# Optimization experiments

Measured on AMD Instinct MI355X. Metric: run time of the kernel, lower is better.

## Reference

```python
import jax, jax.numpy as jnp
import numpy as np

STAGE = 100  # number of weight bins


def _bin_reconstruct(w, affine):
    # Faithful vectorization of the 100-iter binning loop: element in bin i
    # (half-open interval) gets scaled by affine[i]; the max element falls
    # outside every bin (w < wmin + stage*range/stage fails) and is zeroed.
    flat = w.reshape(-1)
    wmin, wmax = flat.min(), flat.max()
    idx = jnp.floor((flat - wmin) / (wmax - wmin) * STAGE).astype(jnp.int32)
    mask = (idx < STAGE).astype(flat.dtype)  # mask is detached in torch (non-diff anyway)
    scale = affine[jnp.clip(idx, 0, STAGE - 1)]
    return flat * scale * mask


def _kl_vs_laplace(new_flat, lap):
    # F.kl_div(log_softmax(w), softmax(lap), reduction='none').mean()
    logq = jax.nn.log_softmax(new_flat)
    p = jax.nn.softmax(lap)
    return (p * (jnp.log(p) - logq)).mean()


def _adder2d(x, w, stride, padding, groups=1):
    # AdderNet conv: out = -sum_k |patch_k - w_k| (no bias)
    O, Cg, kh, kw = w.shape
    patches = jax.lax.conv_general_dilated_patches(
        x, (kh, kw), (stride, stride), [(padding, padding), (padding, padding)])
    B, _, Hp, Wp = patches.shape  # channel dim ordered (C, kh, kw), C-major
    if groups == 1:
        p = patches.reshape(B, 1, Cg * kh * kw, Hp, Wp)
        wf = w.reshape(1, O, Cg * kh * kw, 1, 1)
    else:  # depthwise: groups == C_in, Cg == 1, O == C_in
        p = patches.reshape(B, O, kh * kw, Hp, Wp)
        wf = w.reshape(1, O, kh * kw, 1, 1)
    return -jnp.abs(p - wf).sum(axis=2)  # [B, O, Hp, Wp]


def _bn_train(x, g, b, eps=1e-5):
    # BatchNorm2d in training mode (batch statistics, biased variance)
    m = x.mean(axis=(0, 2, 3), keepdims=True)
    v = ((x - m) ** 2).mean(axis=(0, 2, 3), keepdims=True)
    return (x - m) * jax.lax.rsqrt(v + eps) * g.reshape(1, -1, 1, 1) + b.reshape(1, -1, 1, 1)


def _forward(x, sw_ds, sw_c1, sw_c2, sw_c3, a_ds, a_c1, a_c2, a_c3, peg_w,
             g1, b1, g2, b2, g3, b3, gds, bds, lap_ds, lap_c1, lap_c2, lap_c3):
    kl = jnp.float32(0.0)
    f_ds = _bin_reconstruct(sw_ds, a_ds)
    kl = kl + _kl_vs_laplace(f_ds, lap_ds)
    f_c1 = _bin_reconstruct(sw_c1, a_c1)
    kl = kl + _kl_vs_laplace(f_c1, lap_c1)
    residual = jax.nn.relu(_bn_train(_adder2d(x, f_ds.reshape(sw_ds.shape), 1, 0), gds, bds))
    h = _adder2d(x, f_c1.reshape(sw_c1.shape), 1, 0)
    h = _adder2d(h, peg_w, 1, 1, groups=peg_w.shape[0])  # PEG depthwise 3x3
    h = jax.nn.relu(_bn_train(h, g1, b1))
    f_c2 = _bin_reconstruct(sw_c2, a_c2)
    kl = kl + _kl_vs_laplace(f_c2, lap_c2)
    h = _adder2d(h, f_c2.reshape(sw_c2.shape), 1, 1)
    h = jax.nn.relu(_bn_train(h, g2, b2))
    f_c3 = _bin_reconstruct(sw_c3, a_c3)
    kl = kl + _kl_vs_laplace(f_c3, lap_c3)
    h = _adder2d(h, f_c3.reshape(sw_c3.shape), 1, 0)
    h = _bn_train(h, g3, b3)  # bn3 gamma zero-initialized
    return jax.nn.relu(h + residual), kl


def setup_inputs() -> dict:
    key = jax.random.key(0)
    ks = jax.random.split(key, 16)
    inp = {
        'x': jax.random.normal(ks[0], (4, 128, 28, 28), jnp.float32),
        'sw_downsample': jax.random.normal(ks[1], (256, 128, 1, 1), jnp.float32) * 0.05,
        'sw_conv1': jax.random.normal(ks[2], (64, 128, 1, 1), jnp.float32) * 0.05,
        'sw_conv2': jax.random.normal(ks[3], (64, 64, 3, 3), jnp.float32) * 0.05,
        'sw_conv3': jax.random.normal(ks[4], (256, 64, 1, 1), jnp.float32) * 0.05,
        'downsample_affine': jax.random.normal(ks[5], (100,), jnp.float32),
        'conv1_affine': jax.random.normal(ks[6], (100,), jnp.float32),
        'conv2_affine': jax.random.normal(ks[7], (100,), jnp.float32),
        'conv3_affine': jax.random.normal(ks[8], (100,), jnp.float32),
        'peg_w': jax.random.normal(ks[9], (64, 1, 3, 3), jnp.float32) * 0.05,
        'bn1_g': jnp.ones((64,), jnp.float32), 'bn1_b': jnp.zeros((64,), jnp.float32),
        'bn2_g': jnp.ones((64,), jnp.float32), 'bn2_b': jnp.zeros((64,), jnp.float32),
        'bn3_g': jnp.zeros((256,), jnp.float32), 'bn3_b': jnp.zeros((256,), jnp.float32),
        'bnds_g': jnp.ones((256,), jnp.float32), 'bnds_b': jnp.zeros((256,), jnp.float32),
        # Laplace(0, 2) samples, drawn once in setup so the reference is deterministic
        'lap_ds': jax.random.laplace(ks[10], (32768,), jnp.float32) * 2.0,
        'lap_c1': jax.random.laplace(ks[11], (8192,), jnp.float32) * 2.0,
        'lap_c2': jax.random.laplace(ks[12], (36864,), jnp.float32) * 2.0,
        'lap_c3': jax.random.laplace(ks[13], (16384,), jnp.float32) * 2.0,
    }
    return inp


def reference(x, sw_downsample, sw_conv1, sw_conv2, sw_conv3,
              downsample_affine, conv1_affine, conv2_affine, conv3_affine, peg_w,
              bn1_g, bn1_b, bn2_g, bn2_b, bn3_g, bn3_b, bnds_g, bnds_b,
              lap_ds, lap_c1, lap_c2, lap_c3):
    return _forward(x, sw_downsample, sw_conv1, sw_conv2, sw_conv3,
                    downsample_affine, conv1_affine, conv2_affine, conv3_affine, peg_w,
                    bn1_g, bn1_b, bn2_g, bn2_b, bn3_g, bn3_b, bnds_g, bnds_b,
                    lap_ds, lap_c1, lap_c2, lap_c3)
```

## Files before the change

### kernel.cpp

```cpp
#include <hip/hip_runtime.h>
#include <math.h>


#define HW 784
#define NB 4
#define STAGE 100

__device__ __forceinline__ float wredSum(float v){
  for (int o = 32; o > 0; o >>= 1) v += __shfl_down(v, o, 64);
  return v;
}
__device__ __forceinline__ float wredMax(float v){
  for (int o = 32; o > 0; o >>= 1) v = fmaxf(v, __shfl_down(v, o, 64));
  return v;
}
__device__ __forceinline__ float wredMin(float v){
  for (int o = 32; o > 0; o >>= 1) v = fminf(v, __shfl_down(v, o, 64));
  return v;
}
__device__ __forceinline__ double wredSumD(double v){
  for (int o = 32; o > 0; o >>= 1) v += __shfl_down(v, o, 64);
  return v;
}

__device__ float blockSum16(float v){
  __shared__ float sh[16];
  __syncthreads();
  v = wredSum(v);
  if ((threadIdx.x & 63) == 0) sh[threadIdx.x >> 6] = v;
  __syncthreads();
  float r = 0.0f;
  #pragma unroll
  for (int i = 0; i < 16; i++) r += sh[i];
  return r;
}
__device__ float blockMax16(float v){
  __shared__ float sh[16];
  __syncthreads();
  v = wredMax(v);
  if ((threadIdx.x & 63) == 0) sh[threadIdx.x >> 6] = v;
  __syncthreads();
  float r = sh[0];
  #pragma unroll
  for (int i = 1; i < 16; i++) r = fmaxf(r, sh[i]);
  return r;
}
__device__ float blockMin16(float v){
  __shared__ float sh[16];
  __syncthreads();
  v = wredMin(v);
  if ((threadIdx.x & 63) == 0) sh[threadIdx.x >> 6] = v;
  __syncthreads();
  float r = sh[0];
  #pragma unroll
  for (int i = 1; i < 16; i++) r = fminf(r, sh[i]);
  return r;
}

__device__ void stats4(float v0, float v1, float v2, float v3,
                       double* sumP, double* sqP, int oc0){
  __shared__ double sred[4][8];
  const int w = threadIdx.x >> 6;
  float vv[4] = {v0, v1, v2, v3};
  #pragma unroll
  for (int i = 0; i < 4; i++){
    double d = (double)vv[i];
    double s = wredSumD(d);
    double q = wredSumD(d * d);
    if ((threadIdx.x & 63) == 0){ sred[w][i] = s; sred[w][4 + i] = q; }
  }
  __syncthreads();
  if (threadIdx.x < 8){
    double tot = sred[0][threadIdx.x] + sred[1][threadIdx.x]
               + sred[2][threadIdx.x] + sred[3][threadIdx.x];
    int i = threadIdx.x & 3;
    if (threadIdx.x < 4) atomicAdd(&sumP[oc0 + i], tot);
    else                 atomicAdd(&sqP[oc0 + i],  tot);
  }
}
__device__ void stats2(float v0, float v1, double* sumP, double* sqP, int oc0){
  __shared__ double sred2[4][4];
  const int w = threadIdx.x >> 6;
  float vv[2] = {v0, v1};
  #pragma unroll
  for (int i = 0; i < 2; i++){
    double d = (double)vv[i];
    double s = wredSumD(d);
    double q = wredSumD(d * d);
    if ((threadIdx.x & 63) == 0){ sred2[w][i] = s; sred2[w][2 + i] = q; }
  }
  __syncthreads();
  if (threadIdx.x < 4){
    double tot = sred2[0][threadIdx.x] + sred2[1][threadIdx.x]
               + sred2[2][threadIdx.x] + sred2[3][threadIdx.x];
    int i = threadIdx.x & 1;
    if (threadIdx.x < 2) atomicAdd(&sumP[oc0 + i], tot);
    else                 atomicAdd(&sqP[oc0 + i],  tot);
  }
}

__global__ __launch_bounds__(1024) void recon_kl_kernel(
    const float* w0, const float* a0, const float* l0, float* f0, int n0,
    const float* w1, const float* a1, const float* l1, float* f1, int n1,
    const float* w2, const float* a2, const float* l2, float* f2, int n2,
    const float* w3, const float* a3, const float* l3, float* f3, int n3,
    float* kl_out, double* dstat)
{
  for (int i = threadIdx.x; i < 320; i += 1024) dstat[blockIdx.x * 320 + i] = 0.0;

  const float* w; const float* aff; const float* lap; float* f; int n;
  int t = blockIdx.x;
  if      (t == 0){ w = w0; aff = a0; lap = l0; f = f0; n = n0; }
  else if (t == 1){ w = w1; aff = a1; lap = l1; f = f1; n = n1; }
  else if (t == 2){ w = w2; aff = a2; lap = l2; f = f2; n = n2; }
  else            { w = w3; aff = a3; lap = l3; f = f3; n = n3; }

  __shared__ float saff[STAGE];
  for (int i = threadIdx.x; i < STAGE; i += 1024) saff[i] = aff[i];

  const float4* w4 = (const float4*)w;
  const float4* l4 = (const float4*)lap;
  float4*       f4 = (float4*)f;
  const int n4 = n >> 2;

  float mn = 3.402823466e38f, mx = -3.402823466e38f, ml = -3.402823466e38f;
  for (int i = threadIdx.x; i < n4; i += 1024){
    float4 v = w4[i];
    mn = fminf(mn, fminf(fminf(v.x, v.y), fminf(v.z, v.w)));
    mx = fmaxf(mx, fmaxf(fmaxf(v.x, v.y), fmaxf(v.z, v.w)));
    float4 u = l4[i];
    ml = fmaxf(ml, fmaxf(fmaxf(u.x, u.y), fmaxf(u.z, u.w)));
  }
  mn = blockMin16(mn); mx = blockMax16(mx); ml = blockMax16(ml);
  const float rng = mx - mn;

  float maxf = -3.402823466e38f;
  for (int i = threadIdx.x; i < n4; i += 1024){
    float4 v = w4[i];
    float4 o;
    float* vp = &v.x; float* op = &o.x;
    #pragma unroll
    for (int k = 0; k < 4; k++){
      float vv = vp[k];
      float q = (vv - mn) / rng * 100.0f;
      int idx = (int)floorf(q);
      float nv = 0.0f;
      if (idx < STAGE){
        int ci = idx < 0 ? 0 : (idx > STAGE - 1 ? STAGE - 1 : idx);
        nv = vv * saff[ci];
      }
      op[k] = nv;
      maxf = fmaxf(maxf, nv);
    }
    f4[i] = o;
  }
  maxf = blockMax16(maxf);

  float se = 0.0f, sel = 0.0f, sef = 0.0f, sq = 0.0f;
  for (int i = threadIdx.x; i < n4; i += 1024){
    float4 u = l4[i];
    float4 fv = f4[i];
    float* up = &u.x; float* fp = &fv.x;
    #pragma unroll
    for (int k = 0; k < 4; k++){
      float e = expf(up[k] - ml);
      se  += e;
      sel += e * up[k];
      sef += e * fp[k];
      sq  += expf(fp[k] - maxf);
    }
  }
  se  = blockSum16(se);
  sel = blockSum16(sel);
  sef = blockSum16(sef);
  sq  = blockSum16(sq);

  if (threadIdx.x == 0){
    kl_out[t] = ((sel - sef) / se - ml - logf(se) + maxf + logf(sq)) / (float)n;
  }
}

__global__ __launch_bounds__(256) void front_kernel(
    const float* __restrict__ x, const float* __restrict__ f_ds,
    const float* __restrict__ f_c1, const float* __restrict__ peg_w,
    float* __restrict__ A, float* __restrict__ T2, double* __restrict__ dS)
{
  const int t = threadIdx.x;
  if (blockIdx.x < 1024){
    const int a = blockIdx.x;
    const int chunk = a & 3, og = (a >> 2) & 63, b = a >> 8;
    const int oc0 = og * 4;
    __shared__ float sw[512];
    for (int k = t; k < 512; k += 256) sw[k] = f_ds[oc0 * 128 + k];
    __syncthreads();
    const int px = chunk * 256 + t;
    float v0 = 0, v1 = 0, v2 = 0, v3 = 0;
    if (px < HW){
      const float* xp = x + (size_t)b * 128 * HW + px;
      float c0 = 0, c1 = 0, c2 = 0, c3 = 0;
      #pragma unroll 4
      for (int c = 0; c < 128; c++){
        float xv = xp[(size_t)c * HW];
        c0 += fabsf(xv - sw[c]);
        c1 += fabsf(xv - sw[128 + c]);
        c2 += fabsf(xv - sw[256 + c]);
        c3 += fabsf(xv - sw[384 + c]);
      }
      v0 = -c0; v1 = -c1; v2 = -c2; v3 = -c3;
      float* op = A + ((size_t)(b * 256 + oc0)) * HW + px;
      op[0] = v0; op[HW] = v1; op[2 * HW] = v2; op[3 * HW] = v3;
    }
    stats4(v0, v1, v2, v3, dS + 0, dS + 256, oc0);
  } else {
    const int a = blockIdx.x - 1024;
    const int rc = a & 3, og = (a >> 2) & 15, b = a >> 6;
    const int oc0 = og * 4;
    __shared__ float swc[512];
    __shared__ float swp[36];
    __shared__ float sT1[4][256];
    for (int k = t; k < 512; k += 256) swc[k] = f_c1[oc0 * 128 + k];
    if (t < 36) swp[t] = peg_w[oc0 * 9 + t];
    __syncthreads();
    if (t < 252){
      const int rr = t / 28;
      const int col = t - rr * 28;
      const int wr = rc * 7 - 1 + rr;
      float tv0 = 0, tv1 = 0, tv2 = 0, tv3 = 0;
      if (wr >= 0 && wr < 28){
        const float* xp = x + (size_t)b * 128 * HW + wr * 28 + col;
        float c0 = 0, c1 = 0, c2 = 0, c3 = 0;
        #pragma unroll 4
        for (int c = 0; c < 128; c++){
          float xv = xp[(size_t)c * HW];
          c0 += fabsf(xv - swc[c]);
          c1 += fabsf(xv - swc[128 + c]);
          c2 += fabsf(xv - swc[256 + c]);
          c3 += fabsf(xv - swc[384 + c]);
        }
        tv0 = -c0; tv1 = -c1; tv2 = -c2; tv3 = -c3;
      }
      sT1[0][t] = tv0; sT1[1][t] = tv1; sT1[2][t] = tv2; sT1[3][t] = tv3;
    }
    __syncthreads();
    float v0 = 0, v1 = 0, v2 = 0, v3 = 0;
    if (t < 196){
      const int r = t / 28, col = t - r * 28;
      float c0 = 0, c1 = 0, c2 = 0, c3 = 0;
      #pragma unroll
      for (int ky = 0; ky < 3; ky++){
        #pragma unroll
        for (int kx = 0; kx < 3; kx++){
          int cc = col + kx - 1;
          bool ok = (cc >= 0) && (cc < 28);
          int idx = ok ? ((r + ky) * 28 + cc) : 0;
          float p0 = ok ? sT1[0][idx] : 0.0f;
          float p1 = ok ? sT1[1][idx] : 0.0f;
          float p2 = ok ? sT1[2][idx] : 0.0f;
          float p3 = ok ? sT1[3][idx] : 0.0f;
          int wk = ky * 3 + kx;
          c0 += fabsf(p0 - swp[wk]);
          c1 += fabsf(p1 - swp[9 + wk]);
          c2 += fabsf(p2 - swp[18 + wk]);
          c3 += fabsf(p3 - swp[27 + wk]);
        }
      }
      v0 = -c0; v1 = -c1; v2 = -c2; v3 = -c3;
      const int opx = (rc * 7 + r) * 28 + col;
      float* op = T2 + ((size_t)(b * 64 + oc0)) * HW + opx;
      op[0] = v0; op[HW] = v1; op[2 * HW] = v2; op[3 * HW] = v3;
    }
    stats4(v0, v1, v2, v3, dS + 512, dS + 576, oc0);
  }
}

__global__ __launch_bounds__(256) void mid3x3_kernel(
    const float* __restrict__ T2, const float* __restrict__ f_c2,
    const float* __restrict__ g1, const float* __restrict__ b1,
    float* __restrict__ T3, double* __restrict__ dS)
{
  const int t = threadIdx.x;
  const int a = blockIdx.x;
  const int chunk = a & 3, og = (a >> 2) & 31, b = a >> 7;
  const int oc0 = og * 2;
  __shared__ float ssc[64], ssb[64];
  __shared__ float sw[1152];
  if (t < 64){
    double s  = dS[512 + t] * (1.0 / 3136.0);
    double vr = dS[576 + t] * (1.0 / 3136.0) - s * s;
    float scale = g1[t] * rsqrtf((float)vr + 1e-5f);
    ssc[t] = scale; ssb[t] = b1[t] - (float)s * scale;
  }
  for (int k = t; k < 1152; k += 256) sw[k] = f_c2[oc0 * 576 + k];
  __syncthreads();

  const int px = chunk * 256 + t;
  float v0 = 0, v1 = 0;
  if (px < HW){
    const int y = px / 28, xc = px - y * 28;
    bool val[9]; int off[9];
    #pragma unroll
    for (int ky = 0; ky < 3; ky++){
      #pragma unroll
      for (int kx = 0; kx < 3; kx++){
        int iy = y + ky - 1, ix = xc + kx - 1;
        bool ok = (iy >= 0) && (iy < 28) && (ix >= 0) && (ix < 28);
        val[ky * 3 + kx] = ok;
        off[ky * 3 + kx] = ok ? iy * 28 + ix : 0;
      }
    }
    float c0 = 0, c1 = 0;
    const float* base = T2 + (size_t)b * 64 * HW;
    for (int c = 0; c < 64; c++){
      const float* bc = base + (size_t)c * HW;
      const float sc_ = ssc[c], bi_ = ssb[c];
      const float* w0 = sw + c * 9;
      const float* w1 = sw + 576 + c * 9;
      #pragma unroll
      for (int k = 0; k < 9; k++){
        float raw = val[k] ? bc[off[k]] : 0.0f;
        float vv  = val[k] ? fmaxf(raw * sc_ + bi_, 0.0f) : 0.0f;
        c0 += fabsf(vv - w0[k]);
        c1 += fabsf(vv - w1[k]);
      }
    }
    v0 = -c0; v1 = -c1;
    T3[((size_t)(b * 64 + oc0)) * HW + px]     = v0;
    T3[((size_t)(b * 64 + oc0 + 1)) * HW + px] = v1;
  }
  stats2(v0, v1, dS + 640, dS + 704, oc0);
}

__global__ __launch_bounds__(256) void back_kernel(
    const float* __restrict__ T3, const float* __restrict__ f_c3,
    const float* __restrict__ g2, const float* __restrict__ b2,
    float* __restrict__ out, double* __restrict__ dS)
{
  const int t = threadIdx.x;
  const int a = blockIdx.x;
  const int chunk = a & 3, og = (a >> 2) & 63, b = a >> 8;
  const int oc0 = og * 4;
  __shared__ float ssc[64], ssb[64], sw[256];
  if (t < 64){
    double s  = dS[640 + t] * (1.0 / 3136.0);
    double vr = dS[704 + t] * (1.0 / 3136.0) - s * s;
    float scale = g2[t] * rsqrtf((float)vr + 1e-5f);
    ssc[t] = scale; ssb[t] = b2[t] - (float)s * scale;
  }
  sw[t] = f_c3[oc0 * 64 + t];
  __syncthreads();

  const int px = chunk * 256 + t;
  float v0 = 0, v1 = 0, v2 = 0, v3 = 0;
  if (px < HW){
    const float* bp = T3 + (size_t)b * 64 * HW + px;
    float c0 = 0, c1 = 0, c2 = 0, c3 = 0;
    #pragma unroll 4
    for (int c = 0; c < 64; c++){
      float raw = bp[(size_t)c * HW];
      float vv = fmaxf(raw * ssc[c] + ssb[c], 0.0f);
      c0 += fabsf(vv - sw[c]);
      c1 += fabsf(vv - sw[64 + c]);
      c2 += fabsf(vv - sw[128 + c]);
      c3 += fabsf(vv - sw[192 + c]);
    }
    v0 = -c0; v1 = -c1; v2 = -c2; v3 = -c3;
    float* op = out + ((size_t)(b * 256 + oc0)) * HW + px;
    op[0] = v0; op[HW] = v1; op[2 * HW] = v2; op[3 * HW] = v3;
  }
  stats4(v0, v1, v2, v3, dS + 768, dS + 1024, oc0);
}

__global__ __launch_bounds__(256) void final_kernel(
    float* __restrict__ out, const float* __restrict__ A,
    const float* __restrict__ g3, const float* __restrict__ b3,
    const float* __restrict__ gds, const float* __restrict__ bds,
    const double* __restrict__ dS, const float* __restrict__ kl)
{
  __shared__ float s3c[256], s3b[256], sdc[256], sdb[256];
  const int t = threadIdx.x;
  {
    double s  = dS[768 + t] * (1.0 / 3136.0);
    double vr = dS[1024 + t] * (1.0 / 3136.0) - s * s;
    float scale = g3[t] * rsqrtf((float)vr + 1e-5f);
    s3c[t] = scale; s3b[t] = b3[t] - (float)s * scale;
    s  = dS[t] * (1.0 / 3136.0);
    vr = dS[256 + t] * (1.0 / 3136.0) - s * s;
    scale = gds[t] * rsqrtf((float)vr + 1e-5f);
    sdc[t] = scale; sdb[t] = bds[t] - (float)s * scale;
  }
  __syncthreads();
  #pragma unroll
  for (int k = 0; k < 4; k++){
    int n = blockIdx.x * 1024 + k * 256 + t;
    int c = (n / HW) & 255;
    float h = out[n], aa = A[n];
    float r = fmaxf(aa * sdc[c] + sdb[c], 0.0f);
    out[n] = fmaxf(h * s3c[c] + s3b[c] + r, 0.0f);
  }
  if (blockIdx.x == 0 && t == 0) out[802816] = kl[0] + kl[1] + kl[2] + kl[3];
}

extern "C" void kernel_launch(void* const* d_in, const int* in_sizes, int n_in,
                              void* d_out, int out_size, void* d_ws, size_t ws_size,
                              hipStream_t stream)
{
  const float* x      = (const float*)d_in[0];
  const float* sw_ds  = (const float*)d_in[1];
  const float* sw_c1  = (const float*)d_in[2];
  const float* sw_c2  = (const float*)d_in[3];
  const float* sw_c3  = (const float*)d_in[4];
  const float* a_ds   = (const float*)d_in[5];
  const float* a_c1   = (const float*)d_in[6];
  const float* a_c2   = (const float*)d_in[7];
  const float* a_c3   = (const float*)d_in[8];
  const float* peg_w  = (const float*)d_in[9];
  const float* bn1_g  = (const float*)d_in[10];
  const float* bn1_b  = (const float*)d_in[11];
  const float* bn2_g  = (const float*)d_in[12];
  const float* bn2_b  = (const float*)d_in[13];
  const float* bn3_g  = (const float*)d_in[14];
  const float* bn3_b  = (const float*)d_in[15];
  const float* bnds_g = (const float*)d_in[16];
  const float* bnds_b = (const float*)d_in[17];
  const float* lap_ds = (const float*)d_in[18];
  const float* lap_c1 = (const float*)d_in[19];
  const float* lap_c2 = (const float*)d_in[20];
  const float* lap_c3 = (const float*)d_in[21];

  float* ws    = (float*)d_ws;
  float* f_ds  = ws;
  float* f_c1  = ws + 32768;
  float* f_c2  = ws + 40960;
  float* f_c3  = ws + 77824;
  float* kl    = ws + 94208;
  double* dstat= (double*)(ws + 98304);
  float* A     = ws + 102400;
  float* T2    = ws + 905216;
  float* T3    = ws + 1105920;

  float* out = (float*)d_out;

  recon_kl_kernel<<<4, 1024, 0, stream>>>(
      sw_ds, a_ds, lap_ds, f_ds, 32768,
      sw_c1, a_c1, lap_c1, f_c1, 8192,
      sw_c2, a_c2, lap_c2, f_c2, 36864,
      sw_c3, a_c3, lap_c3, f_c3, 16384, kl, dstat);

  front_kernel<<<1280, 256, 0, stream>>>(x, f_ds, f_c1, peg_w, A, T2, dstat);

  mid3x3_kernel<<<512, 256, 0, stream>>>(T2, f_c2, bn1_g, bn1_b, T3, dstat);

  back_kernel<<<1024, 256, 0, stream>>>(T3, f_c3, bn2_g, bn2_b, out, dstat);

  final_kernel<<<784, 256, 0, stream>>>(out, A, bn3_g, bn3_b, bnds_g, bnds_b,
                                        dstat, kl);
}
```

Measured before the change: 204.5 us.

## Precompute BN+ReLU into padded buffer for 3x3 adder conv, widen downsample tiles

Adds a kernel that applies the BN1 scale/shift and ReLU once into a zero-padded 32-wide buffer. The 3x3 adder conv then reads this buffer without bounds checks or per-tap BN math, and reads its weights straight from global memory instead of shared memory. The downsample branch of the front kernel now computes 8 output channels per block instead of 4, halving the block count and reusing each x load across more channels. A leading __syncthreads is added to the stats helpers so their shared buffers are safe to reuse. In exchange there is an extra launch and an extra padded buffer to write and read.

After: 188.2 us. -8.0%, faster.

```diff
diff --git a/kernel.cpp b/kernel.cpp
--- a/kernel.cpp
+++ b/kernel.cpp
@@ -60,6 +60,7 @@
 __device__ void stats4(float v0, float v1, float v2, float v3,
                        double* sumP, double* sqP, int oc0){
   __shared__ double sred[4][8];
+  __syncthreads();
   const int w = threadIdx.x >> 6;
   float vv[4] = {v0, v1, v2, v3};
   #pragma unroll
@@ -80,6 +81,7 @@
 }
 __device__ void stats2(float v0, float v1, double* sumP, double* sqP, int oc0){
   __shared__ double sred2[4][4];
+  __syncthreads();
   const int w = threadIdx.x >> 6;
   float vv[2] = {v0, v1};
   #pragma unroll
@@ -186,18 +188,18 @@
     float* __restrict__ A, float* __restrict__ T2, double* __restrict__ dS)
 {
   const int t = threadIdx.x;
-  if (blockIdx.x < 1024){
+  if (blockIdx.x < 512){
     const int a = blockIdx.x;
-    const int chunk = a & 3, og = (a >> 2) & 63, b = a >> 8;
-    const int oc0 = og * 4;
-    __shared__ float sw[512];
-    for (int k = t; k < 512; k += 256) sw[k] = f_ds[oc0 * 128 + k];
+    const int chunk = a & 3, og = (a >> 2) & 31, b = a >> 7;
+    const int oc0 = og * 8;
+    __shared__ float sw[1024];
+    for (int k = t; k < 1024; k += 256) sw[k] = f_ds[oc0 * 128 + k];
     __syncthreads();
     const int px = chunk * 256 + t;
-    float v0 = 0, v1 = 0, v2 = 0, v3 = 0;
+    float v0=0,v1=0,v2=0,v3=0,v4=0,v5=0,v6=0,v7=0;
     if (px < HW){
       const float* xp = x + (size_t)b * 128 * HW + px;
-      float c0 = 0, c1 = 0, c2 = 0, c3 = 0;
+      float c0=0,c1=0,c2=0,c3=0,c4=0,c5=0,c6=0,c7=0;
       #pragma unroll 4
       for (int c = 0; c < 128; c++){
         float xv = xp[(size_t)c * HW];
@@ -205,14 +207,20 @@
         c1 += fabsf(xv - sw[128 + c]);
         c2 += fabsf(xv - sw[256 + c]);
         c3 += fabsf(xv - sw[384 + c]);
+        c4 += fabsf(xv - sw[512 + c]);
+        c5 += fabsf(xv - sw[640 + c]);
+        c6 += fabsf(xv - sw[768 + c]);
+        c7 += fabsf(xv - sw[896 + c]);
       }
-      v0 = -c0; v1 = -c1; v2 = -c2; v3 = -c3;
+      v0=-c0; v1=-c1; v2=-c2; v3=-c3; v4=-c4; v5=-c5; v6=-c6; v7=-c7;
       float* op = A + ((size_t)(b * 256 + oc0)) * HW + px;
-      op[0] = v0; op[HW] = v1; op[2 * HW] = v2; op[3 * HW] = v3;
+      op[0]=v0; op[HW]=v1; op[2*HW]=v2; op[3*HW]=v3;
+      op[4*HW]=v4; op[5*HW]=v5; op[6*HW]=v6; op[7*HW]=v7;
     }
     stats4(v0, v1, v2, v3, dS + 0, dS + 256, oc0);
+    stats4(v4, v5, v6, v7, dS + 0, dS + 256, oc0 + 4);
   } else {
-    const int a = blockIdx.x - 1024;
+    const int a = blockIdx.x - 512;
     const int rc = a & 3, og = (a >> 2) & 15, b = a >> 6;
     const int oc0 = og * 4;
     __shared__ float swc[512];
@@ -273,55 +281,64 @@
   }
 }
 
+__global__ __launch_bounds__(256) void bnapply_pad_kernel(
+    const float* __restrict__ T2, float* __restrict__ T2b,
+    const float* __restrict__ g1, const float* __restrict__ b1,
+    const double* __restrict__ dS)
+{
+  const int a = blockIdx.x;
+  const int c = a & 63, b = a >> 6;
+  __shared__ float ssc, ssb;
+  if (threadIdx.x == 0){
+    double s  = dS[512 + c] * (1.0 / 3136.0);
+    double vr = dS[576 + c] * (1.0 / 3136.0) - s * s;
+    float scale = g1[c] * rsqrtf((float)vr + 1e-5f);
+    ssc = scale; ssb = b1[c] - (float)s * scale;
+  }
+  __syncthreads();
+  const float sc_ = ssc, bi_ = ssb;
+  const float* src = T2 + (size_t)a * HW;
+  float* dst = T2b + (size_t)a * 960;
+  for (int i = threadIdx.x; i < 960; i += 256){
+    int row = i >> 5, col = i & 31;
+    float v = 0.0f;
+    if (row >= 1 && row <= 28 && col >= 1 && col <= 28)
+      v = fmaxf(src[(row - 1) * 28 + (col - 1)] * sc_ + bi_, 0.0f);
+    dst[i] = v;
+  }
+}
+
 __global__ __launch_bounds__(256) void mid3x3_kernel(
-    const float* __restrict__ T2, const float* __restrict__ f_c2,
-    const float* __restrict__ g1, const float* __restrict__ b1,
+    const float* __restrict__ T2b, const float* __restrict__ f_c2,
     float* __restrict__ T3, double* __restrict__ dS)
 {
   const int t = threadIdx.x;
   const int a = blockIdx.x;
   const int chunk = a & 3, og = (a >> 2) & 31, b = a >> 7;
   const int oc0 = og * 2;
-  __shared__ float ssc[64], ssb[64];
-  __shared__ float sw[1152];
-  if (t < 64){
-    double s  = dS[512 + t] * (1.0 / 3136.0);
-    double vr = dS[576 + t] * (1.0 / 3136.0) - s * s;
-    float scale = g1[t] * rsqrtf((float)vr + 1e-5f);
-    ssc[t] = scale; ssb[t] = b1[t] - (float)s * scale;
-  }
-  for (int k = t; k < 1152; k += 256) sw[k] = f_c2[oc0 * 576 + k];
-  __syncthreads();
-
-  const int px = chunk * 256 + t;
+  const float* __restrict__ wA = f_c2 + oc0 * 576;
+  const float* __restrict__ wB = wA + 576;
+
   float v0 = 0, v1 = 0;
-  if (px < HW){
+  const int px = chunk * 196 + t;
+  if (t < 196){
     const int y = px / 28, xc = px - y * 28;
-    bool val[9]; int off[9];
-    #pragma unroll
-    for (int ky = 0; ky < 3; ky++){
-      #pragma unroll
-      for (int kx = 0; kx < 3; kx++){
-        int iy = y + ky - 1, ix = xc + kx - 1;
-        bool ok = (iy >= 0) && (iy < 28) && (ix >= 0) && (ix < 28);
-        val[ky * 3 + kx] = ok;
-        off[ky * 3 + kx] = ok ? iy * 28 + ix : 0;
-      }
-    }
+    const float* base = T2b + (size_t)b * 64 * 960 + y * 32 + xc;
     float c0 = 0, c1 = 0;
-    const float* base = T2 + (size_t)b * 64 * HW;
+    #pragma unroll 2
     for (int c = 0; c < 64; c++){
-      const float* bc = base + (size_t)c * HW;
-      const float sc_ = ssc[c], bi_ = ssb[c];
-      const float* w0 = sw + c * 9;
-      const float* w1 = sw + 576 + c * 9;
-      #pragma unroll
-      for (int k = 0; k < 9; k++){
-        float raw = val[k] ? bc[off[k]] : 0.0f;
-        float vv  = val[k] ? fmaxf(raw * sc_ + bi_, 0.0f) : 0.0f;
-        c0 += fabsf(vv - w0[k]);
-        c1 += fabsf(vv - w1[k]);
-      }
+      const float* p = base + c * 960;
+      float t0 = p[0],  t1 = p[1],  t2 = p[2];
+      float t3 = p[32], t4 = p[33], t5 = p[34];
+      float t6 = p[64], t7 = p[65], t8 = p[66];
+      const float* wa = wA + c * 9;
+      const float* wb = wB + c * 9;
+      c0 += fabsf(t0 - wa[0]) + fabsf(t1 - wa[1]) + fabsf(t2 - wa[2])
+          + fabsf(t3 - wa[3]) + fabsf(t4 - wa[4]) + fabsf(t5 - wa[5])
+          + fabsf(t6 - wa[6]) + fabsf(t7 - wa[7]) + fabsf(t8 - wa[8]);
+      c1 += fabsf(t0 - wb[0]) + fabsf(t1 - wb[1]) + fabsf(t2 - wb[2])
+          + fabsf(t3 - wb[3]) + fabsf(t4 - wb[4]) + fabsf(t5 - wb[5])
+          + fabsf(t6 - wb[6]) + fabsf(t7 - wb[7]) + fabsf(t8 - wb[8]);
     }
     v0 = -c0; v1 = -c1;
     T3[((size_t)(b * 64 + oc0)) * HW + px]     = v0;
@@ -437,6 +454,7 @@
   float* A     = ws + 102400;
   float* T2    = ws + 905216;
   float* T3    = ws + 1105920;
+  float* T2b   = ws + 1306624;
 
   float* out = (float*)d_out;
 
@@ -446,9 +464,11 @@
       sw_c2, a_c2, lap_c2, f_c2, 36864,
       sw_c3, a_c3, lap_c3, f_c3, 16384, kl, dstat);
 
-  front_kernel<<<1280, 256, 0, stream>>>(x, f_ds, f_c1, peg_w, A, T2, dstat);
-
-  mid3x3_kernel<<<512, 256, 0, stream>>>(T2, f_c2, bn1_g, bn1_b, T3, dstat);
+  front_kernel<<<768, 256, 0, stream>>>(x, f_ds, f_c1, peg_w, A, T2, dstat);
+
+  bnapply_pad_kernel<<<256, 256, 0, stream>>>(T2, T2b, bn1_g, bn1_b, dstat);
+
+  mid3x3_kernel<<<512, 256, 0, stream>>>(T2b, f_c2, T3, dstat);
 
   back_kernel<<<1024, 256, 0, stream>>>(T3, f_c3, bn2_g, bn2_b, out, dstat);
 
```
